# Kernel tuning notes

Measured on AMD Instinct MI355X. Metric: run time of the kernel, lower is better.

Reference implementation:

```python
import jax, jax.numpy as jnp
import numpy as np

N_NODES = 8192
N_EDGES = 262144
D_IN = 512
D_OUT = 512


def setup_inputs() -> dict:
    key = jax.random.key(0)
    k1, k2, k3 = jax.random.split(key, 3)
    x = jax.random.normal(k1, (N_NODES, D_IN), dtype=jnp.float32)
    edge_index = jax.random.randint(k2, (2, N_EDGES), 0, N_NODES, dtype=jnp.int64)
    weight = jax.random.normal(k3, (D_IN, D_OUT), dtype=jnp.float32)
    bias = jnp.zeros((D_OUT,), dtype=jnp.float32)
    return {"x": x, "edge_index": edge_index, "weight": weight, "bias": bias}


def reference(x, edge_index, weight, bias):
    # GCN layer with selfloop=True branch of the original module.
    n = x.shape[0]
    # Dense symmetric adjacency via scatter-set, matching adj[ei0,ei1]=1; adj[ei1,ei0]=1
    adj = jnp.zeros((n, n), dtype=x.dtype)
    adj = adj.at[edge_index[0], edge_index[1]].set(1.0)
    adj = adj.at[edge_index[1], edge_index[0]].set(1.0)
    # Add self loops, symmetric degree normalization D^{-1/2} A D^{-1/2}
    adj = adj + jnp.eye(n, dtype=x.dtype)
    deg = jnp.sum(adj, axis=1)
    dinv = 1.0 / jnp.sqrt(deg)
    adj = adj * dinv[:, None] * dinv[None, :]  # == D @ adj @ D (diagonal scaling)
    return adj @ (x @ weight) + bias
```

## Files before the change

### kernel.cpp

```cpp
#include <hip/hip_runtime.h>
#include <hip/hip_bf16.h>


#define ELL_STRIDE 128

typedef __attribute__((ext_vector_type(8))) short bf16x8;
typedef __attribute__((ext_vector_type(4))) float f32x4;

__device__ __forceinline__ unsigned short f2bf(float f) {
  unsigned u = __float_as_uint(f);
  u = (u + 0x7fff + ((u >> 16) & 1)) >> 16;
  return (unsigned short)u;
}
__device__ __forceinline__ float bflo(unsigned u) {
  return __uint_as_float(u << 16);
}
__device__ __forceinline__ float bfhi(unsigned u) {
  return __uint_as_float(u & 0xffff0000u);
}

__global__ __launch_bounds__(256) void fused_front_kernel(
    const int* __restrict__ ei, unsigned* __restrict__ mask, int n_edges,
    int words,
    const float* __restrict__ x, unsigned short* __restrict__ xb, int n4,
    const float* __restrict__ W, unsigned short* __restrict__ Wt, int K, int N,
    unsigned short* __restrict__ Hs, float* __restrict__ dinv, int n_nodes,
    int edge_blocks, int cast_blocks, int tr_blocks) {
  const int bid = blockIdx.x;
  if (bid < edge_blocks) {
    const int e = bid * 256 + threadIdx.x;
    if (e < n_edges) {
      const int u = ei[e];
      const int v = ei[e + n_edges];
      atomicOr(&mask[(size_t)u * words + (v >> 5)], 1u << (v & 31));
      atomicOr(&mask[(size_t)v * words + (u >> 5)], 1u << (u & 31));
    }
    return;
  }
  if (bid < edge_blocks + cast_blocks) {
    const int t = (bid - edge_blocks) * 256 + threadIdx.x;
    if (t < n4) {
      float4 v = ((const float4*)x)[t];
      ushort4 o;
      o.x = f2bf(v.x); o.y = f2bf(v.y); o.z = f2bf(v.z); o.w = f2bf(v.w);
      ((ushort4*)xb)[t] = o;
    }
    return;
  }
  if (bid < edge_blocks + cast_blocks + tr_blocks) {
    __shared__ float tile[32][33];
    const int b = bid - edge_blocks - cast_blocks;
    const int bx = b & ((N >> 5) - 1);
    const int by = b >> (31 - __builtin_clz(N >> 5));
    const int tx = threadIdx.x & 31;
    const int ty = threadIdx.x >> 5;
#pragma unroll
    for (int r = 0; r < 4; ++r)
      tile[ty + 8 * r][tx] = W[(size_t)(by * 32 + ty + 8 * r) * N + bx * 32 + tx];
    __syncthreads();
#pragma unroll
    for (int r = 0; r < 4; ++r)
      Wt[(size_t)(bx * 32 + ty + 8 * r) * K + by * 32 + tx] =
          f2bf(tile[tx][ty + 8 * r]);
    return;
  }
  {
    const int t = threadIdx.x;
    if (t < (N >> 1)) ((unsigned*)(Hs + (size_t)n_nodes * N))[t] = 0;
    if (t == 0) dinv[n_nodes] = 0.f;
  }
}

__global__ __launch_bounds__(256) void fused_mid_kernel(
    const unsigned short* __restrict__ xb,
    const unsigned short* __restrict__ Wt,
    unsigned short* __restrict__ Hs,
    const unsigned* __restrict__ mask, unsigned short* __restrict__ ell,
    int* __restrict__ deg, float* __restrict__ dinv,
    int M, int N, int K, int words, int gemm_blocks, int nbx_sh) {
  __shared__ unsigned short As[512 * 8];
  __shared__ unsigned short Bs[512 * 8];

  const int tid = threadIdx.x;
  const int bid = blockIdx.x;

  if (bid < gemm_blocks) {
    const int wave = tid >> 6;
    const int lane = tid & 63;
    const int q = lane >> 4;
    const int c = lane & 15;
    const int bx = bid & ((1 << nbx_sh) - 1);
    const int by = bid >> nbx_sh;
    const int m0 = by * 64;
    const int n0 = bx * 64;
    const int wr = wave >> 1, wc = wave & 1;

    f32x4 acc[2][2] = {};

    for (int k0 = 0; k0 < K; k0 += 64) {
#pragma unroll
      for (int t = 0; t < 2; ++t) {
        const int sbase = t * 256 + wave * 64;
        const int s = sbase + lane;
        const unsigned short* g =
            xb + (size_t)(m0 + (s & 63)) * K + k0 + (s >> 6) * 8;
        __builtin_amdgcn_global_load_lds(
            (const __attribute__((address_space(1))) void*)g,
            (__attribute__((address_space(3))) void*)(As + sbase * 8), 16, 0, 0);
      }
#pragma unroll
      for (int t = 0; t < 2; ++t) {
        const int sbase = t * 256 + wave * 64;
        const int s = sbase + lane;
        const unsigned short* g =
            Wt + (size_t)(n0 + (s >> 3)) * K + k0 + (s & 7) * 8;
        __builtin_amdgcn_global_load_lds(
            (const __attribute__((address_space(1))) void*)g,
            (__attribute__((address_space(3))) void*)(Bs + sbase * 8), 16, 0, 0);
      }
      __syncthreads();

#pragma unroll
      for (int kk = 0; kk < 2; ++kk) {
        bf16x8 a[2], b[2];
#pragma unroll
        for (int tm = 0; tm < 2; ++tm) {
          const int row = wr * 32 + tm * 16 + c;
          a[tm] = *(const bf16x8*)(As + (((kk * 4 + q) * 64) + row) * 8);
        }
#pragma unroll
        for (int tn = 0; tn < 2; ++tn) {
          const int n = wc * 32 + tn * 16 + c;
          b[tn] = *(const bf16x8*)(Bs + (n * 8 + kk * 4 + q) * 8);
        }
#pragma unroll
        for (int tm = 0; tm < 2; ++tm)
#pragma unroll
          for (int tn = 0; tn < 2; ++tn)
            acc[tm][tn] = __builtin_amdgcn_mfma_f32_16x16x32_bf16(
                a[tm], b[tn], acc[tm][tn], 0, 0, 0);
      }
      __syncthreads();
    }

#pragma unroll
    for (int tm = 0; tm < 2; ++tm) {
#pragma unroll
      for (int r = 0; r < 4; ++r) {
        const int grow = m0 + wr * 32 + tm * 16 + q * 4 + r;
#pragma unroll
        for (int tn = 0; tn < 2; ++tn) {
          const int gcol = n0 + wc * 32 + tn * 16 + c;
          Hs[(size_t)grow * N + gcol] = f2bf(acc[tm][tn][r]);
        }
      }
    }
    return;
  }

  {
    const int wave = tid >> 6, lane = tid & 63;
    const int node = (bid - gemm_blocks) * 4 + wave;
    const unsigned* __restrict__ row = mask + (size_t)node * words;
    unsigned short* __restrict__ out = ell + (size_t)node * ELL_STRIDE;

    int running = 0;
    for (int r = 0; r < words; r += 64) {
      const int w = r + lane;
      unsigned bits = row[w];
      const int cnt = __popc(bits);
      int x = cnt;
#pragma unroll
      for (int d = 1; d < 64; d <<= 1) {
        int y = __shfl_up(x, d, 64);
        if (lane >= d) x += y;
      }
      int pos = running + x - cnt;
      while (bits) {
        const int b = __builtin_ctz(bits);
        bits &= bits - 1;
        if (pos < ELL_STRIDE) out[pos] = (unsigned short)((w << 5) + b);
        ++pos;
      }
      running += __shfl(x, 63, 64);
    }
    for (int p = running + lane; p < ELL_STRIDE; p += 64)
      out[p] = (unsigned short)(p == running ? node : M);
    if (lane == 0) {
      const int dd = running + 1;
      deg[node] = dd < ELL_STRIDE ? dd : ELL_STRIDE;
      dinv[node] = rsqrtf((float)running + 1.0f);
    }
  }
}

__global__ __launch_bounds__(256) void spmm_kernel(
    const unsigned short* __restrict__ ell, const int* __restrict__ deg,
    const float* __restrict__ dinv, const unsigned short* __restrict__ Hs,
    const float* __restrict__ bias, float* __restrict__ out, int n, int D) {
  __shared__ uint2 ji[4][ELL_STRIDE];
  const int wave = threadIdx.x >> 6, lane = threadIdx.x & 63;
  const int i = blockIdx.x * 4 + wave;
  const int h = blockIdx.y;
  const int side = lane >> 5, hl = lane & 31;
  const int Dh = D >> 1;

  {
    const unsigned j0 = ell[(size_t)i * ELL_STRIDE + lane];
    const unsigned j1 = ell[(size_t)i * ELL_STRIDE + 64 + lane];
    ji[wave][lane] = make_uint2(j0, __float_as_uint(dinv[j0]));
    ji[wave][64 + lane] = make_uint2(j1, __float_as_uint(dinv[j1]));
  }
  const int d = deg[i];
  const float di = dinv[i];
  const int kmax = (d + 1) & ~1;

  const unsigned short* __restrict__ hb = Hs + h * Dh + hl * 8;
  float acc[8] = {0.f, 0.f, 0.f, 0.f, 0.f, 0.f, 0.f, 0.f};

#pragma unroll 8
  for (int k = 0; k < kmax; k += 2) {
    const uint2 e = ji[wave][k + side];
    const int j = e.x;
    const float dj = __uint_as_float(e.y);
    const uint4 hv = *(const uint4*)(hb + (size_t)j * D);
    acc[0] += dj * bflo(hv.x); acc[1] += dj * bfhi(hv.x);
    acc[2] += dj * bflo(hv.y); acc[3] += dj * bfhi(hv.y);
    acc[4] += dj * bflo(hv.z); acc[5] += dj * bfhi(hv.z);
    acc[6] += dj * bflo(hv.w); acc[7] += dj * bfhi(hv.w);
  }
#pragma unroll
  for (int t = 0; t < 8; ++t) acc[t] += __shfl_xor(acc[t], 32, 64);

  if (side == 0) {
    const float4 b0 = *(const float4*)(bias + h * Dh + hl * 8);
    const float4 b1 = *(const float4*)(bias + h * Dh + hl * 8 + 4);
    float* op = out + (size_t)i * D + h * Dh + hl * 8;
    float4 o0, o1;
    o0.x = di * acc[0] + b0.x; o0.y = di * acc[1] + b0.y;
    o0.z = di * acc[2] + b0.z; o0.w = di * acc[3] + b0.w;
    o1.x = di * acc[4] + b1.x; o1.y = di * acc[5] + b1.y;
    o1.z = di * acc[6] + b1.z; o1.w = di * acc[7] + b1.w;
    *(float4*)op = o0;
    *(float4*)(op + 4) = o1;
  }
}

extern "C" void kernel_launch(void* const* d_in, const int* in_sizes, int n_in,
                              void* d_out, int out_size, void* d_ws, size_t ws_size,
                              hipStream_t stream) {
  const float* x    = (const float*)d_in[0];
  const int*   ei   = (const int*)d_in[1];
  const float* W    = (const float*)d_in[2];
  const float* bias = (const float*)d_in[3];
  float* out = (float*)d_out;

  const int d_out_dim = in_sizes[3];
  const int d_in_dim  = in_sizes[2] / d_out_dim;
  const int n_nodes   = in_sizes[0] / d_in_dim;
  const int n_edges   = in_sizes[1] / 2;
  const int words     = (n_nodes + 31) / 32;

  char* ws = (char*)d_ws;
  size_t off = 0;
  unsigned* mask = (unsigned*)(ws + off); off += (size_t)n_nodes * words * 4;
  int* deg       = (int*)(ws + off);      off += (size_t)n_nodes * 4;
  float* dinv    = (float*)(ws + off);    off += (size_t)(n_nodes + 1) * 4;
  unsigned short* ell = (unsigned short*)(ws + off); off += (size_t)n_nodes * ELL_STRIDE * 2;
  unsigned short* xb  = (unsigned short*)(ws + off); off += (size_t)n_nodes * d_in_dim * 2;
  unsigned short* Wt  = (unsigned short*)(ws + off); off += (size_t)d_in_dim * d_out_dim * 2;
  unsigned short* Hs  = (unsigned short*)(ws + off);
  off += (size_t)(n_nodes + 1) * d_out_dim * 2;

  hipMemsetAsync(mask, 0, (size_t)n_nodes * words * 4, stream);

  const int edge_blocks = (n_edges + 255) / 256;
  const int n4 = n_nodes * d_in_dim / 4;
  const int cast_blocks = (n4 + 255) / 256;
  const int tr_blocks = (d_in_dim / 32) * (d_out_dim / 32);
  fused_front_kernel<<<edge_blocks + cast_blocks + tr_blocks + 1, 256, 0, stream>>>(
      ei, mask, n_edges, words, x, xb, n4, W, Wt, d_in_dim, d_out_dim,
      Hs, dinv, n_nodes, edge_blocks, cast_blocks, tr_blocks);

  const int nbx = d_out_dim / 64;
  const int nbx_sh = 31 - __builtin_clz(nbx);
  const int gemm_blocks = nbx * (n_nodes / 64);
  const int ell_blocks = n_nodes / 4;
  fused_mid_kernel<<<gemm_blocks + ell_blocks, 256, 0, stream>>>(
      xb, Wt, Hs, mask, ell, deg, dinv,
      n_nodes, d_out_dim, d_in_dim, words, gemm_blocks, nbx_sh);

  dim3 sgrid(n_nodes / 4, 2);
  spmm_kernel<<<sgrid, 256, 0, stream>>>(ell, deg, dinv, Hs, bias, out,
                                         n_nodes, d_out_dim);
}
```

Measured before the change: 157.7 us.

## Enlarge GEMM tiles to 128x128 with K-step 32 and schedule ELL blocks first

The GEMM part of the fused mid kernel now computes a 128x128 output tile per block with 4x4 MFMA accumulators per wave and a K step of 32 instead of 64. Shared memory size is unchanged, but each element loaded from global memory feeds more MFMAs, which cuts global traffic and block count. Block order is also flipped so the ELL-building blocks come first and the fewer, heavier GEMM blocks follow. The costs are more accumulator registers, possibly lower occupancy, and twice as many barrier pairs along K.

After: 169.0 us. +7.2%, slower.

```diff
diff --git a/kernel.cpp b/kernel.cpp
--- a/kernel.cpp
+++ b/kernel.cpp
@@ -77,80 +77,78 @@
     unsigned short* __restrict__ Hs,
     const unsigned* __restrict__ mask, unsigned short* __restrict__ ell,
     int* __restrict__ deg, float* __restrict__ dinv,
-    int M, int N, int K, int words, int gemm_blocks, int nbx_sh) {
+    int M, int N, int K, int words, int ell_blocks, int nbx_sh) {
   __shared__ unsigned short As[512 * 8];
   __shared__ unsigned short Bs[512 * 8];
 
   const int tid = threadIdx.x;
   const int bid = blockIdx.x;
 
-  if (bid < gemm_blocks) {
+  if (bid >= ell_blocks) {
+    const int gb = bid - ell_blocks;
     const int wave = tid >> 6;
     const int lane = tid & 63;
     const int q = lane >> 4;
     const int c = lane & 15;
-    const int bx = bid & ((1 << nbx_sh) - 1);
-    const int by = bid >> nbx_sh;
-    const int m0 = by * 64;
-    const int n0 = bx * 64;
+    const int bx = gb & ((1 << nbx_sh) - 1);
+    const int by = gb >> nbx_sh;
+    const int m0 = by * 128;
+    const int n0 = bx * 128;
     const int wr = wave >> 1, wc = wave & 1;
 
-    f32x4 acc[2][2] = {};
-
-    for (int k0 = 0; k0 < K; k0 += 64) {
+    f32x4 acc[4][4] = {};
+
+    for (int k0 = 0; k0 < K; k0 += 32) {
 #pragma unroll
       for (int t = 0; t < 2; ++t) {
-        const int sbase = t * 256 + wave * 64;
+        const int sbase = wave * 128 + t * 64;
         const int s = sbase + lane;
-        const unsigned short* g =
-            xb + (size_t)(m0 + (s & 63)) * K + k0 + (s >> 6) * 8;
+        const int kc = s >> 7, row = s & 127;
+        const unsigned short* g = xb + (size_t)(m0 + row) * K + k0 + kc * 8;
         __builtin_amdgcn_global_load_lds(
             (const __attribute__((address_space(1))) void*)g,
             (__attribute__((address_space(3))) void*)(As + sbase * 8), 16, 0, 0);
       }
 #pragma unroll
       for (int t = 0; t < 2; ++t) {
-        const int sbase = t * 256 + wave * 64;
+        const int sbase = wave * 128 + t * 64;
         const int s = sbase + lane;
-        const unsigned short* g =
-            Wt + (size_t)(n0 + (s >> 3)) * K + k0 + (s & 7) * 8;
+        const int n = s >> 2, kc = s & 3;
+        const unsigned short* g = Wt + (size_t)(n0 + n) * K + k0 + kc * 8;
         __builtin_amdgcn_global_load_lds(
             (const __attribute__((address_space(1))) void*)g,
             (__attribute__((address_space(3))) void*)(Bs + sbase * 8), 16, 0, 0);
       }
       __syncthreads();
 
-#pragma unroll
-      for (int kk = 0; kk < 2; ++kk) {
-        bf16x8 a[2], b[2];
-#pragma unroll
-        for (int tm = 0; tm < 2; ++tm) {
-          const int row = wr * 32 + tm * 16 + c;
-          a[tm] = *(const bf16x8*)(As + (((kk * 4 + q) * 64) + row) * 8);
-        }
-#pragma unroll
-        for (int tn = 0; tn < 2; ++tn) {
-          const int n = wc * 32 + tn * 16 + c;
-          b[tn] = *(const bf16x8*)(Bs + (n * 8 + kk * 4 + q) * 8);
-        }
-#pragma unroll
-        for (int tm = 0; tm < 2; ++tm)
-#pragma unroll
-          for (int tn = 0; tn < 2; ++tn)
-            acc[tm][tn] = __builtin_amdgcn_mfma_f32_16x16x32_bf16(
-                a[tm], b[tn], acc[tm][tn], 0, 0, 0);
-      }
+      bf16x8 a[4], b[4];
+#pragma unroll
+      for (int tm = 0; tm < 4; ++tm) {
+        const int row = wr * 64 + tm * 16 + c;
+        a[tm] = *(const bf16x8*)(As + (q * 128 + row) * 8);
+      }
+#pragma unroll
+      for (int tn = 0; tn < 4; ++tn) {
+        const int n = wc * 64 + tn * 16 + c;
+        b[tn] = *(const bf16x8*)(Bs + (n * 4 + q) * 8);
+      }
+#pragma unroll
+      for (int tm = 0; tm < 4; ++tm)
+#pragma unroll
+        for (int tn = 0; tn < 4; ++tn)
+          acc[tm][tn] = __builtin_amdgcn_mfma_f32_16x16x32_bf16(
+              a[tm], b[tn], acc[tm][tn], 0, 0, 0);
       __syncthreads();
     }
 
 #pragma unroll
-    for (int tm = 0; tm < 2; ++tm) {
+    for (int tm = 0; tm < 4; ++tm) {
 #pragma unroll
       for (int r = 0; r < 4; ++r) {
-        const int grow = m0 + wr * 32 + tm * 16 + q * 4 + r;
-#pragma unroll
-        for (int tn = 0; tn < 2; ++tn) {
-          const int gcol = n0 + wc * 32 + tn * 16 + c;
+        const int grow = m0 + wr * 64 + tm * 16 + q * 4 + r;
+#pragma unroll
+        for (int tn = 0; tn < 4; ++tn) {
+          const int gcol = n0 + wc * 64 + tn * 16 + c;
           Hs[(size_t)grow * N + gcol] = f2bf(acc[tm][tn][r]);
         }
       }
@@ -160,7 +158,7 @@
 
   {
     const int wave = tid >> 6, lane = tid & 63;
-    const int node = (bid - gemm_blocks) * 4 + wave;
+    const int node = bid * 4 + wave;
     const unsigned* __restrict__ row = mask + (size_t)node * words;
     unsigned short* __restrict__ out = ell + (size_t)node * ELL_STRIDE;
 
@@ -282,13 +280,13 @@
       ei, mask, n_edges, words, x, xb, n4, W, Wt, d_in_dim, d_out_dim,
       Hs, dinv, n_nodes, edge_blocks, cast_blocks, tr_blocks);
 
-  const int nbx = d_out_dim / 64;
+  const int nbx = d_out_dim / 128;
   const int nbx_sh = 31 - __builtin_clz(nbx);
-  const int gemm_blocks = nbx * (n_nodes / 64);
+  const int gemm_blocks = nbx * (n_nodes / 128);
   const int ell_blocks = n_nodes / 4;
-  fused_mid_kernel<<<gemm_blocks + ell_blocks, 256, 0, stream>>>(
+  fused_mid_kernel<<<ell_blocks + gemm_blocks, 256, 0, stream>>>(
       xb, Wt, Hs, mask, ell, deg, dinv,
-      n_nodes, d_out_dim, d_in_dim, words, gemm_blocks, nbx_sh);
+      n_nodes, d_out_dim, d_in_dim, words, ell_blocks, nbx_sh);
 
   dim3 sgrid(n_nodes / 4, 2);
   spmm_kernel<<<sgrid, 256, 0, stream>>>(ell, deg, dinv, Hs, bias, out,
```
